# Performance work log

Hardware: AMD Instinct MI355X
Metric: run time of the kernel (lower is better)

Reference implementation:

```python
import jax, jax.numpy as jnp
import numpy as np

B, Q, A, D, H = 64, 16, 4096, 128, 8
HD = D // H
FF = 512

def _layernorm(x, g, b, eps=1e-5):
    mu = jnp.mean(x, axis=-1, keepdims=True)
    var = jnp.var(x, axis=-1, keepdims=True)
    return (x - mu) * jax.lax.rsqrt(var + eps) * g + b

def setup_inputs() -> dict:
    key = jax.random.key(0)
    ks = jax.random.split(key, 8)
    s = 0.05  # weight scale for sane numerics
    return {
        'q': jax.random.normal(ks[0], (B, Q, D), jnp.float32),
        'embed': jax.random.normal(ks[1], (B, A, D), jnp.float32),
        'attn_mask': jnp.zeros((B, Q, A), jnp.bool_),
        'batch_mask': jax.random.randint(ks[2], (B,), 0, B, jnp.int32),
        'W_kv': jax.random.normal(ks[3], (2 * D, D), jnp.float32) * s,
        'W_q': jax.random.normal(ks[4], (D, D), jnp.float32) * s,
        'W_o': jax.random.normal(ks[5], (D, D), jnp.float32) * s,
        'ln1_g': jnp.ones((D,), jnp.float32),
        'ln1_b': jnp.zeros((D,), jnp.float32),
        'ln2_g': jnp.ones((D,), jnp.float32),
        'ln2_b': jnp.zeros((D,), jnp.float32),
        'alpha1': jnp.full((1,), 0.1, jnp.float32),
        'alpha2': jnp.full((1,), 0.1, jnp.float32),
        'w_ff': jax.random.normal(ks[6], (2 * FF, D), jnp.float32) * s,
        'b_ff': jnp.zeros((2 * FF,), jnp.float32),
        'w_ff_out': jax.random.normal(ks[7], (D, FF), jnp.float32) * s,
        'b_ff_out': jnp.zeros((D,), jnp.float32),
    }

def reference(q, embed, attn_mask, batch_mask, W_kv, W_q, W_o,
              ln1_g, ln1_b, ln2_g, ln2_b, alpha1, alpha2,
              w_ff, b_ff, w_ff_out, b_ff_out):
    # cache_keys: project city embeddings to K/V, split into heads
    kv = embed @ W_kv.T                      # [B, A, 2D]
    k, v = jnp.split(kv, 2, axis=-1)
    k = k.reshape(B, A, H, HD).transpose(0, 2, 1, 3)   # [B, H, A, HD]
    v = v.reshape(B, A, H, HD).transpose(0, 2, 1, 3)   # [B, H, A, HD]

    # pre-norm query projection
    q_norm = _layernorm(q, ln1_g, ln1_b)
    gq = (q_norm @ W_q.T).reshape(B, Q, H, HD).transpose(0, 2, 1, 3)  # [B, H, Q, HD]

    # batch gather on cached K/V
    k = k[batch_mask]
    v = v[batch_mask]

    score = jnp.einsum('bhqd,bhkd->bhqk', gq, k) / jnp.sqrt(jnp.float32(HD))
    score = jnp.where(attn_mask[:, None, :, :], -jnp.inf, score)
    attn = jax.nn.softmax(score, axis=-1)
    ctx = jnp.einsum('bhqk,bhkd->bhqd', attn, v)        # [B, H, Q, HD]
    ctx = ctx.transpose(0, 2, 1, 3).reshape(B, Q, D)
    att_out = ctx @ W_o.T

    hidden = q + alpha1 * att_out
    hn = _layernorm(hidden, ln2_g, ln2_b)
    ab = hn @ w_ff.T + b_ff                              # [B, Q, 2*FF]
    a, b = jnp.split(ab, 2, axis=-1)
    h = jax.nn.silu(a) * b
    ff_out = h @ w_ff_out.T + b_ff_out
    return hidden + alpha2 * ff_out
```

## Files before the change

### kernel.cpp

```cpp
#include <hip/hip_runtime.h>
#include <cstdint>
#include <cstddef>

#define B_ 64
#define Q_ 16
#define A_ 4096
#define D_ 128
#define H_ 8
#define HD_ 16
#define FF_ 512
#define NCHUNK 8
#define CHUNK 512
#define GQ_SCALE 0.36067376022224085f

typedef __attribute__((ext_vector_type(4))) float f32x4;
typedef __attribute__((ext_vector_type(8))) __bf16 bf16x8;
typedef __attribute__((ext_vector_type(4))) short s16x4;

static __device__ __forceinline__ short f2bf(float f) {
    __bf16 h = (__bf16)f;
    return __builtin_bit_cast(short, h);
}

static __device__ __forceinline__ f32x4 mfma32(bf16x8 a, bf16x8 b, f32x4 c) {
    return __builtin_amdgcn_mfma_f32_16x16x32_bf16(a, b, c, 0, 0, 0);
}

static __device__ __forceinline__ bf16x8 wfrag_load(const float* p) {
    float4 a = *(const float4*)p;
    float4 b = *(const float4*)(p + 4);
    bf16x8 r;
    r[0]=(__bf16)a.x; r[1]=(__bf16)a.y; r[2]=(__bf16)a.z; r[3]=(__bf16)a.w;
    r[4]=(__bf16)b.x; r[5]=(__bf16)b.y; r[6]=(__bf16)b.z; r[7]=(__bf16)b.w;
    return r;
}

__global__ __launch_bounds__(128) void kgq(
    const float* __restrict__ qin, const float* __restrict__ g1,
    const float* __restrict__ b1, const float* __restrict__ Wq,
    short* __restrict__ gq)
{
    __shared__ float sx[128];
    __shared__ float red[2];
    int r = blockIdx.x;
    int t = threadIdx.x;
    float x = qin[(size_t)r * 128 + t];
    float v = x;
    for (int o = 32; o > 0; o >>= 1) v += __shfl_down(v, o);
    if ((t & 63) == 0) red[t >> 6] = v;
    __syncthreads();
    float mu = (red[0] + red[1]) * (1.f / 128.f);
    __syncthreads();
    float d = x - mu;
    v = d * d;
    for (int o = 32; o > 0; o >>= 1) v += __shfl_down(v, o);
    if ((t & 63) == 0) red[t >> 6] = v;
    __syncthreads();
    float var = (red[0] + red[1]) * (1.f / 128.f);
    float xn = d * rsqrtf(var + 1e-5f) * g1[t] + b1[t];
    sx[t] = xn;
    __syncthreads();
    float acc = 0.f;
    const float4* wr = (const float4*)(Wq + (size_t)t * 128);
    const float4* xv = (const float4*)sx;
    for (int i = 0; i < 32; ++i) {
        float4 a = wr[i], bb = xv[i];
        acc += a.x * bb.x + a.y * bb.y + a.z * bb.z + a.w * bb.w;
    }
    gq[(size_t)r * 128 + t] = f2bf(acc * GQ_SCALE);
}

__global__ __launch_bounds__(256, 2) void kattn(
    const float* __restrict__ embed, const int* __restrict__ bmask,
    const unsigned char* __restrict__ amask, const float* __restrict__ Wkv,
    const short* __restrict__ gq, float* __restrict__ pml,
    float* __restrict__ pctx)
{
    __shared__ __align__(16) short lds[32768];
    const int KR  = 8192;
    const int VR  = 16384;
    const int PR  = 24576;
    const int MK  = 28672;

    const int chunk = blockIdx.x;
    const int b     = blockIdx.y;
    const int t = threadIdx.x;
    const int w = t >> 6;
    const int l = t & 63;
    const int g = l >> 4;
    const int c = l & 15;
    const int s = bmask[b];
    const int a0 = chunk * CHUNK;

    {
        unsigned char* mlb = (unsigned char*)&lds[MK];
        int qr = t >> 5, off = (t & 31) * 16;
        for (int p = 0; p < 2; ++p) {
            int qq = qr + p * 8;
            *(uint4*)&mlb[qq * 512 + off] =
                *(const uint4*)&amask[((size_t)(b * 16 + qq)) * 4096 + a0 + off];
        }
    }

    const bool kw = (w < 2);
    const int wrow0 = kw ? (w * 64) : (128 + (w - 2) * 64);
    bf16x8 wf[4][4];
    for (int xf = 0; xf < 4; ++xf)
        for (int kf = 0; kf < 4; ++kf)
            wf[xf][kf] = wfrag_load(Wkv + (size_t)(wrow0 + xf * 16 + c) * 128
                                        + kf * 32 + g * 8);

    bf16x8 gqA[2];
    for (int hh = 0; hh < 2; ++hh) {
        int h = 2 * w + hh;
        if (g < 2)
            gqA[hh] = *(const bf16x8*)(const void*)
                      (gq + ((size_t)(b * 16 + c)) * 128 + h * 16 + g * 8);
        else {
            bf16x8 z = {};
            gqA[hh] = z;
        }
    }

    f32x4 ctx[2];
    float mrun[2][4], lrun[2][4];
    for (int hh = 0; hh < 2; ++hh)
        for (int r = 0; r < 4; ++r) {
            ctx[hh][r] = 0.f; mrun[hh][r] = -3.0e38f; lrun[hh][r] = 0.f;
        }

    const float* esrc = embed + ((size_t)s * 4096 + a0) * 128;
    const int srow = t >> 5;
    const int scol = (t & 31) * 4;

    float4 pf[8];
    auto loadregs = [&](int ts) {
        for (int p = 0; p < 8; ++p) {
            int rr = srow + p * 8;
            pf[p] = *(const float4*)(esrc + (size_t)(ts * 64 + rr) * 128 + scol);
        }
    };
    loadregs(0);

    for (int ts = 0; ts < 8; ++ts) {
        __syncthreads();
        for (int p = 0; p < 8; ++p) {
            int rr = srow + p * 8;
            int byte = (rr * 256 + scol * 2) ^ ((rr & 7) << 4);
            s16x4 pk;
            pk[0] = f2bf(pf[p].x); pk[1] = f2bf(pf[p].y);
            pk[2] = f2bf(pf[p].z); pk[3] = f2bf(pf[p].w);
            *(s16x4*)(void*)((char*)lds + byte) = pk;
        }
        if (ts < 7) loadregs(ts + 1);
        __syncthreads();
        for (int kb4 = 0; kb4 < 4; ++kb4) {
            bf16x8 eb[4];
            for (int kf = 0; kf < 4; ++kf) {
                int rr = kb4 * 16 + c;
                int byte = (rr * 256 + kf * 64 + g * 16) ^ ((rr & 7) << 4);
                eb[kf] = *(const bf16x8*)(const void*)((char*)lds + byte);
            }
            for (int xf = 0; xf < 4; ++xf) {
                f32x4 acc = {0.f, 0.f, 0.f, 0.f};
                if (kw) { for (int kf = 0; kf < 4; ++kf) acc = mfma32(wf[xf][kf], eb[kf], acc); }
                else    { for (int kf = 0; kf < 4; ++kf) acc = mfma32(eb[kf], wf[xf][kf], acc); }
                s16x4 pk;
                pk[0] = f2bf(acc[0]); pk[1] = f2bf(acc[1]);
                pk[2] = f2bf(acc[2]); pk[3] = f2bf(acc[3]);
                if (kw) {
                    int h = w * 4 + xf;
                    int e = (h * 4 + kb4) * 256 + (g >> 1) * 128 + c * 8 + (g & 1) * 4;
                    *(s16x4*)(void*)&lds[KR + e] = pk;
                } else {
                    int h = (w - 2) * 4 + xf;
                    int e = (h * 2 + (kb4 >> 1)) * 512
                          + ((2 * (kb4 & 1) + (g >> 1)) * 16 + c) * 8 + (g & 1) * 4;
                    *(s16x4*)(void*)&lds[VR + e] = pk;
                }
            }
        }
        __syncthreads();
        float mb[4][4];
        {
            const unsigned char* mlb = (const unsigned char*)&lds[MK];
            for (int kb = 0; kb < 4; ++kb)
                for (int r = 0; r < 4; ++r)
                    mb[kb][r] = mlb[(4 * g + r) * 512 + ts * 64 + kb * 16 + c]
                                ? -1.0e30f : 0.0f;
        }
        for (int hh = 0; hh < 2; ++hh) {
            int h = 2 * w + hh;
            f32x4 sc[4];
            for (int kb = 0; kb < 4; ++kb) {
                bf16x8 kB = *(const bf16x8*)(const void*)
                            &lds[KR + (h * 4 + kb) * 256 + (g * 16 + c) * 8];
                f32x4 z = {0.f, 0.f, 0.f, 0.f};
                sc[kb] = mfma32(gqA[hh], kB, z);
            }
            float al[4], rs[4];
            for (int r = 0; r < 4; ++r) {
                float s0 = sc[0][r] + mb[0][r], s1 = sc[1][r] + mb[1][r];
                float s2 = sc[2][r] + mb[2][r], s3 = sc[3][r] + mb[3][r];
                sc[0][r] = s0; sc[1][r] = s1; sc[2][r] = s2; sc[3][r] = s3;
                float tm = fmaxf(fmaxf(s0, s1), fmaxf(s2, s3));
                for (int o = 1; o < 16; o <<= 1) tm = fmaxf(tm, __shfl_xor(tm, o));
                float mn = fmaxf(mrun[hh][r], tm);
                al[r] = exp2f(mrun[hh][r] - mn);
                mrun[hh][r] = mn;
            }
            for (int r = 0; r < 4; ++r) {
                float p0 = exp2f(sc[0][r] - mrun[hh][r]);
                float p1 = exp2f(sc[1][r] - mrun[hh][r]);
                float p2 = exp2f(sc[2][r] - mrun[hh][r]);
                float p3 = exp2f(sc[3][r] - mrun[hh][r]);
                sc[0][r] = p0; sc[1][r] = p1; sc[2][r] = p2; sc[3][r] = p3;
                float qsum = p0 + p1 + p2 + p3;
                for (int o = 1; o < 16; o <<= 1) qsum += __shfl_xor(qsum, o);
                rs[r] = qsum;
            }
            for (int r = 0; r < 4; ++r) {
                lrun[hh][r] = lrun[hh][r] * al[r] + rs[r];
                ctx[hh][r] *= al[r];
            }
            for (int kb = 0; kb < 4; ++kb) {
                int base = PR + w * 1024 + (kb >> 1) * 512;
                int khi = 2 * (kb & 1) + (c >> 3);
                for (int r = 0; r < 4; ++r)
                    lds[base + (khi * 16 + 4 * g + r) * 8 + (c & 7)] = f2bf(sc[kb][r]);
            }
            for (int k2 = 0; k2 < 2; ++k2) {
                bf16x8 pA = *(const bf16x8*)(const void*)
                            &lds[PR + w * 1024 + k2 * 512 + (g * 16 + c) * 8];
                bf16x8 vB = *(const bf16x8*)(const void*)
                            &lds[VR + (h * 2 + k2) * 512 + (g * 16 + c) * 8];
                ctx[hh] = mfma32(pA, vB, ctx[hh]);
            }
        }
    }
    for (int hh = 0; hh < 2; ++hh) {
        int h = 2 * w + hh;
        size_t base = (((size_t)b * 8 + h) * 8 + chunk) * 16;
        for (int r = 0; r < 4; ++r)
            pctx[(base + 4 * g + r) * 16 + c] = ctx[hh][r];
        if (c == 0) {
            for (int r = 0; r < 4; ++r) {
                pml[(base + 4 * g + r) * 2 + 0] = mrun[hh][r];
                pml[(base + 4 * g + r) * 2 + 1] = lrun[hh][r];
            }
        }
    }
}

__global__ __launch_bounds__(128) void kcomb(
    const float* __restrict__ pml, const float* __restrict__ pctx,
    const float* __restrict__ Wo, const float* __restrict__ qin,
    const float* __restrict__ alpha1, const float* __restrict__ g2,
    const float* __restrict__ b2, float* __restrict__ hidden,
    short* __restrict__ hn)
{
    __shared__ float scx[128];
    __shared__ float red[2];
    int r = blockIdx.x;
    int b = r >> 4, qq = r & 15;
    int d = threadIdx.x;
    int h = d >> 4, vd = d & 15;
    size_t mlb = (((size_t)b * 8 + h) * 8) * 32 + qq * 2;
    float M = -3.0e38f;
    for (int cc = 0; cc < 8; ++cc) M = fmaxf(M, pml[mlb + cc * 32]);
    float L = 0.f, cx = 0.f;
    for (int cc = 0; cc < 8; ++cc) {
        float mm = pml[mlb + cc * 32], ll = pml[mlb + cc * 32 + 1];
        float f = exp2f(mm - M);
        L += ll * f;
        cx += pctx[((((size_t)b * 8 + h) * 8 + cc) * 16 + qq) * 16 + vd] * f;
    }
    cx /= L;
    scx[d] = cx;
    __syncthreads();
    float ao = 0.f;
    const float4* wo = (const float4*)(Wo + (size_t)d * 128);
    const float4* xv = (const float4*)scx;
    for (int i = 0; i < 32; ++i) {
        float4 a = wo[i], bb = xv[i];
        ao += a.x * bb.x + a.y * bb.y + a.z * bb.z + a.w * bb.w;
    }
    float hid = qin[(size_t)r * 128 + d] + alpha1[0] * ao;
    hidden[(size_t)r * 128 + d] = hid;
    float v = hid;
    for (int o = 32; o > 0; o >>= 1) v += __shfl_down(v, o);
    if ((d & 63) == 0) red[d >> 6] = v;
    __syncthreads();
    float mu = (red[0] + red[1]) * (1.f / 128.f);
    __syncthreads();
    float dd = hid - mu;
    v = dd * dd;
    for (int o = 32; o > 0; o >>= 1) v += __shfl_down(v, o);
    if ((d & 63) == 0) red[d >> 6] = v;
    __syncthreads();
    float var = (red[0] + red[1]) * (1.f / 128.f);
    hn[(size_t)r * 128 + d] = f2bf(dd * rsqrtf(var + 1e-5f) * g2[d] + b2[d]);
}

__global__ __launch_bounds__(256) void kff(
    const short* __restrict__ hn, const float* __restrict__ wff,
    const float* __restrict__ bff, const float* __restrict__ wffo,
    float* __restrict__ ffp)
{
    __shared__ float abm[2][16][132];
    __shared__ __align__(16) short hm[16 * 136];
    int b = blockIdx.x >> 2, jt = blockIdx.x & 3;
    int t = threadIdx.x, w = t >> 6, l = t & 63, g = l >> 4, c = l & 15;
    (void)l;
    bf16x8 ha[4];
    for (int kf = 0; kf < 4; ++kf)
        ha[kf] = *(const bf16x8*)(const void*)
                 (hn + ((size_t)b * 16 + c) * 128 + kf * 32 + g * 8);
    int isb = w >> 1, colb = (w & 1) * 64;
    for (int nf = 0; nf < 4; ++nf) {
        f32x4 acc = {0.f, 0.f, 0.f, 0.f};
        int lcol = colb + nf * 16 + c;
        int wrow = isb * 512 + jt * 128 + lcol;
        for (int kf = 0; kf < 4; ++kf) {
            bf16x8 wb = wfrag_load(wff + (size_t)wrow * 128 + kf * 32 + g * 8);
            acc = mfma32(ha[kf], wb, acc);
        }
        float bias = bff[wrow];
        for (int r = 0; r < 4; ++r) abm[isb][4 * g + r][lcol] = acc[r] + bias;
    }
    __syncthreads();
    for (int it = 0; it < 8; ++it) {
        int e = it * 256 + t, qq = e >> 7, jj = e & 127;
        float a = abm[0][qq][jj], bb = abm[1][qq][jj];
        float hv = a * bb / (1.f + __expf(-a));
        hm[qq * 136 + jj] = f2bf(hv);
    }
    __syncthreads();
    bf16x8 hf[4];
    for (int kf = 0; kf < 4; ++kf)
        hf[kf] = *(const bf16x8*)(const void*)&hm[c * 136 + kf * 32 + g * 8];
    for (int nf = 0; nf < 2; ++nf) {
        f32x4 a2 = {0.f, 0.f, 0.f, 0.f};
        int dout = w * 32 + nf * 16 + c;
        for (int kf = 0; kf < 4; ++kf) {
            bf16x8 wb = wfrag_load(wffo + (size_t)dout * 512 + jt * 128
                                        + kf * 32 + g * 8);
            a2 = mfma32(hf[kf], wb, a2);
        }
        for (int r = 0; r < 4; ++r)
            ffp[((size_t)jt * 1024 + b * 16 + 4 * g + r) * 128 + dout] = a2[r];
    }
}

__global__ __launch_bounds__(256) void kout(
    const float* __restrict__ hidden, const float* __restrict__ ffp,
    const float* __restrict__ bffo, const float* __restrict__ alpha2,
    float* __restrict__ out)
{
    int i = blockIdx.x * 256 + threadIdx.x;
    float f = ffp[i] + ffp[131072 + i] + ffp[262144 + i] + ffp[393216 + i]
            + bffo[i & 127];
    out[i] = hidden[i] + alpha2[0] * f;
}

extern "C" void kernel_launch(void* const* d_in, const int* in_sizes, int n_in,
                              void* d_out, int out_size, void* d_ws, size_t ws_size,
                              hipStream_t stream)
{
    (void)in_sizes; (void)n_in; (void)out_size; (void)ws_size;
    const float* qin   = (const float*)d_in[0];
    const float* embed = (const float*)d_in[1];
    const unsigned char* amask = (const unsigned char*)d_in[2];
    const int*   bmask = (const int*)d_in[3];
    const float* Wkv   = (const float*)d_in[4];
    const float* Wq    = (const float*)d_in[5];
    const float* Wo    = (const float*)d_in[6];
    const float* g1    = (const float*)d_in[7];
    const float* b1    = (const float*)d_in[8];
    const float* g2    = (const float*)d_in[9];
    const float* b2    = (const float*)d_in[10];
    const float* al1   = (const float*)d_in[11];
    const float* al2   = (const float*)d_in[12];
    const float* wff   = (const float*)d_in[13];
    const float* bff   = (const float*)d_in[14];
    const float* wffo  = (const float*)d_in[15];
    const float* bffo  = (const float*)d_in[16];
    float* out = (float*)d_out;

    char* ws = (char*)d_ws;
    short* gqb  = (short*)(ws + 0);
    short* hnb  = (short*)(ws + 262144);
    float* hid  = (float*)(ws + 524288);
    float* pml  = (float*)(ws + 1048576);
    float* pctx = (float*)(ws + 1572864);
    float* ffp  = (float*)(ws + 5767168);

    kgq  <<<dim3(1024),   dim3(128), 0, stream>>>(qin, g1, b1, Wq, gqb);
    kattn<<<dim3(8, 64),  dim3(256), 0, stream>>>(embed, bmask, amask, Wkv,
                                                  gqb, pml, pctx);
    kcomb<<<dim3(1024),   dim3(128), 0, stream>>>(pml, pctx, Wo, qin, al1,
                                                  g2, b2, hid, hnb);
    kff  <<<dim3(256),    dim3(256), 0, stream>>>(hnb, wff, bff, wffo, ffp);
    kout <<<dim3(512),    dim3(256), 0, stream>>>(hid, ffp, bffo, al2, out);
}
```

Before: 274.7 us.

## Pre-convert weights to bf16, widen attention blocks, fuse combine/FFN/output tail

Adds a prep kernel that converts all weight matrices to bf16 once per call, so the consumer kernels no longer redo the fp32-to-bf16 conversion per fragment. The attention kernel goes to 512 threads, with one wave per head and smaller per-thread register and prefetch state. The split-softmax combine, Wo projection, second layernorm, both FFN matmuls and the output epilogue are merged into a single 64-block tail kernel, removing the global round-trips for hidden, hn and the FFN partial sums. The trade-off is that the tail runs on only 64 blocks, and there is one extra small kernel launch.

```diff
diff --git a/kernel.cpp b/kernel.cpp
--- a/kernel.cpp
+++ b/kernel.cpp
@@ -9,8 +9,6 @@
 #define H_ 8
 #define HD_ 16
 #define FF_ 512
-#define NCHUNK 8
-#define CHUNK 512
 #define GQ_SCALE 0.36067376022224085f
 
 typedef __attribute__((ext_vector_type(4))) float f32x4;
@@ -26,13 +24,22 @@
     return __builtin_amdgcn_mfma_f32_16x16x32_bf16(a, b, c, 0, 0, 0);
 }
 
-static __device__ __forceinline__ bf16x8 wfrag_load(const float* p) {
-    float4 a = *(const float4*)p;
-    float4 b = *(const float4*)(p + 4);
-    bf16x8 r;
-    r[0]=(__bf16)a.x; r[1]=(__bf16)a.y; r[2]=(__bf16)a.z; r[3]=(__bf16)a.w;
-    r[4]=(__bf16)b.x; r[5]=(__bf16)b.y; r[6]=(__bf16)b.z; r[7]=(__bf16)b.w;
-    return r;
+__global__ __launch_bounds__(256) void kprep(
+    const float* __restrict__ wkv, const float* __restrict__ wo,
+    const float* __restrict__ wff, const float* __restrict__ wffo,
+    short* __restrict__ o_kv, short* __restrict__ o_wo,
+    short* __restrict__ o_ff, short* __restrict__ o_ffo)
+{
+    int i = (blockIdx.x * 256 + threadIdx.x) * 4;
+    const float* src; short* dst; int off;
+    if (i < 32768)       { src = wkv;  dst = o_kv;  off = i; }
+    else if (i < 49152)  { src = wo;   dst = o_wo;  off = i - 32768; }
+    else if (i < 180224) { src = wff;  dst = o_ff;  off = i - 49152; }
+    else                 { src = wffo; dst = o_ffo; off = i - 180224; }
+    float4 v = *(const float4*)(src + off);
+    s16x4 p;
+    p[0] = f2bf(v.x); p[1] = f2bf(v.y); p[2] = f2bf(v.z); p[3] = f2bf(v.w);
+    *(s16x4*)(dst + off) = p;
 }
 
 __global__ __launch_bounds__(128) void kgq(
@@ -70,17 +77,17 @@
     gq[(size_t)r * 128 + t] = f2bf(acc * GQ_SCALE);
 }
 
-__global__ __launch_bounds__(256, 2) void kattn(
+__global__ __launch_bounds__(512, 4) void kattn(
     const float* __restrict__ embed, const int* __restrict__ bmask,
-    const unsigned char* __restrict__ amask, const float* __restrict__ Wkv,
+    const unsigned char* __restrict__ amask, const short* __restrict__ wkv16,
     const short* __restrict__ gq, float* __restrict__ pml,
     float* __restrict__ pctx)
 {
-    __shared__ __align__(16) short lds[32768];
+    __shared__ __align__(16) short lds[36864];
     const int KR  = 8192;
     const int VR  = 16384;
     const int PR  = 24576;
-    const int MK  = 28672;
+    const int MK  = 32768;
 
     const int chunk = blockIdx.x;
     const int b     = blockIdx.y;
@@ -90,62 +97,50 @@
     const int g = l >> 4;
     const int c = l & 15;
     const int s = bmask[b];
-    const int a0 = chunk * CHUNK;
+    const int a0 = chunk * 512;
 
     {
         unsigned char* mlb = (unsigned char*)&lds[MK];
         int qr = t >> 5, off = (t & 31) * 16;
-        for (int p = 0; p < 2; ++p) {
-            int qq = qr + p * 8;
-            *(uint4*)&mlb[qq * 512 + off] =
-                *(const uint4*)&amask[((size_t)(b * 16 + qq)) * 4096 + a0 + off];
-        }
-    }
-
-    const bool kw = (w < 2);
-    const int wrow0 = kw ? (w * 64) : (128 + (w - 2) * 64);
-    bf16x8 wf[4][4];
-    for (int xf = 0; xf < 4; ++xf)
+        *(uint4*)&mlb[qr * 512 + off] =
+            *(const uint4*)&amask[((size_t)(b * 16 + qr)) * 4096 + a0 + off];
+    }
+
+    const bool kw = (w < 4);
+    const int wrow0 = kw ? (w * 32) : (128 + (w - 4) * 32);
+    bf16x8 wf[2][4];
+    for (int xf = 0; xf < 2; ++xf)
         for (int kf = 0; kf < 4; ++kf)
-            wf[xf][kf] = wfrag_load(Wkv + (size_t)(wrow0 + xf * 16 + c) * 128
-                                        + kf * 32 + g * 8);
-
-    bf16x8 gqA[2];
-    for (int hh = 0; hh < 2; ++hh) {
-        int h = 2 * w + hh;
-        if (g < 2)
-            gqA[hh] = *(const bf16x8*)(const void*)
-                      (gq + ((size_t)(b * 16 + c)) * 128 + h * 16 + g * 8);
-        else {
-            bf16x8 z = {};
-            gqA[hh] = z;
-        }
-    }
-
-    f32x4 ctx[2];
-    float mrun[2][4], lrun[2][4];
-    for (int hh = 0; hh < 2; ++hh)
-        for (int r = 0; r < 4; ++r) {
-            ctx[hh][r] = 0.f; mrun[hh][r] = -3.0e38f; lrun[hh][r] = 0.f;
-        }
+            wf[xf][kf] = *(const bf16x8*)(const void*)
+                         (wkv16 + (size_t)(wrow0 + xf * 16 + c) * 128
+                                + kf * 32 + g * 8);
+
+    bf16x8 gqA;
+    if (g < 2)
+        gqA = *(const bf16x8*)(const void*)
+              (gq + ((size_t)(b * 16 + c)) * 128 + w * 16 + g * 8);
+    else { bf16x8 z = {}; gqA = z; }
+
+    f32x4 ctx = {0.f, 0.f, 0.f, 0.f};
+    float mrun[4], lrun[4];
+    for (int r = 0; r < 4; ++r) { mrun[r] = -3.0e38f; lrun[r] = 0.f; }
 
     const float* esrc = embed + ((size_t)s * 4096 + a0) * 128;
     const int srow = t >> 5;
     const int scol = (t & 31) * 4;
 
-    float4 pf[8];
+    float4 pf[4];
     auto loadregs = [&](int ts) {
-        for (int p = 0; p < 8; ++p) {
-            int rr = srow + p * 8;
-            pf[p] = *(const float4*)(esrc + (size_t)(ts * 64 + rr) * 128 + scol);
-        }
+        for (int p = 0; p < 4; ++p)
+            pf[p] = *(const float4*)(esrc + (size_t)(ts * 64 + srow + p * 16) * 128
+                                     + scol);
     };
     loadregs(0);
 
     for (int ts = 0; ts < 8; ++ts) {
         __syncthreads();
-        for (int p = 0; p < 8; ++p) {
-            int rr = srow + p * 8;
+        for (int p = 0; p < 4; ++p) {
+            int rr = srow + p * 16;
             int byte = (rr * 256 + scol * 2) ^ ((rr & 7) << 4);
             s16x4 pk;
             pk[0] = f2bf(pf[p].x); pk[1] = f2bf(pf[p].y);
@@ -161,7 +156,7 @@
                 int byte = (rr * 256 + kf * 64 + g * 16) ^ ((rr & 7) << 4);
                 eb[kf] = *(const bf16x8*)(const void*)((char*)lds + byte);
             }
-            for (int xf = 0; xf < 4; ++xf) {
+            for (int xf = 0; xf < 2; ++xf) {
                 f32x4 acc = {0.f, 0.f, 0.f, 0.f};
                 if (kw) { for (int kf = 0; kf < 4; ++kf) acc = mfma32(wf[xf][kf], eb[kf], acc); }
                 else    { for (int kf = 0; kf < 4; ++kf) acc = mfma32(eb[kf], wf[xf][kf], acc); }
@@ -169,11 +164,11 @@
                 pk[0] = f2bf(acc[0]); pk[1] = f2bf(acc[1]);
                 pk[2] = f2bf(acc[2]); pk[3] = f2bf(acc[3]);
                 if (kw) {
-                    int h = w * 4 + xf;
+                    int h = 2 * w + xf;
                     int e = (h * 4 + kb4) * 256 + (g >> 1) * 128 + c * 8 + (g & 1) * 4;
                     *(s16x4*)(void*)&lds[KR + e] = pk;
                 } else {
-                    int h = (w - 2) * 4 + xf;
+                    int h = 2 * (w - 4) + xf;
                     int e = (h * 2 + (kb4 >> 1)) * 512
                           + ((2 * (kb4 & 1) + (g >> 1)) * 16 + c) * 8 + (g & 1) * 4;
                     *(s16x4*)(void*)&lds[VR + e] = pk;
@@ -189,178 +184,195 @@
                     mb[kb][r] = mlb[(4 * g + r) * 512 + ts * 64 + kb * 16 + c]
                                 ? -1.0e30f : 0.0f;
         }
-        for (int hh = 0; hh < 2; ++hh) {
-            int h = 2 * w + hh;
-            f32x4 sc[4];
-            for (int kb = 0; kb < 4; ++kb) {
-                bf16x8 kB = *(const bf16x8*)(const void*)
-                            &lds[KR + (h * 4 + kb) * 256 + (g * 16 + c) * 8];
-                f32x4 z = {0.f, 0.f, 0.f, 0.f};
-                sc[kb] = mfma32(gqA[hh], kB, z);
-            }
-            float al[4], rs[4];
-            for (int r = 0; r < 4; ++r) {
-                float s0 = sc[0][r] + mb[0][r], s1 = sc[1][r] + mb[1][r];
-                float s2 = sc[2][r] + mb[2][r], s3 = sc[3][r] + mb[3][r];
-                sc[0][r] = s0; sc[1][r] = s1; sc[2][r] = s2; sc[3][r] = s3;
-                float tm = fmaxf(fmaxf(s0, s1), fmaxf(s2, s3));
-                for (int o = 1; o < 16; o <<= 1) tm = fmaxf(tm, __shfl_xor(tm, o));
-                float mn = fmaxf(mrun[hh][r], tm);
-                al[r] = exp2f(mrun[hh][r] - mn);
-                mrun[hh][r] = mn;
-            }
-            for (int r = 0; r < 4; ++r) {
-                float p0 = exp2f(sc[0][r] - mrun[hh][r]);
-                float p1 = exp2f(sc[1][r] - mrun[hh][r]);
-                float p2 = exp2f(sc[2][r] - mrun[hh][r]);
-                float p3 = exp2f(sc[3][r] - mrun[hh][r]);
-                sc[0][r] = p0; sc[1][r] = p1; sc[2][r] = p2; sc[3][r] = p3;
-                float qsum = p0 + p1 + p2 + p3;
-                for (int o = 1; o < 16; o <<= 1) qsum += __shfl_xor(qsum, o);
-                rs[r] = qsum;
-            }
-            for (int r = 0; r < 4; ++r) {
-                lrun[hh][r] = lrun[hh][r] * al[r] + rs[r];
-                ctx[hh][r] *= al[r];
-            }
-            for (int kb = 0; kb < 4; ++kb) {
-                int base = PR + w * 1024 + (kb >> 1) * 512;
-                int khi = 2 * (kb & 1) + (c >> 3);
-                for (int r = 0; r < 4; ++r)
-                    lds[base + (khi * 16 + 4 * g + r) * 8 + (c & 7)] = f2bf(sc[kb][r]);
-            }
-            for (int k2 = 0; k2 < 2; ++k2) {
-                bf16x8 pA = *(const bf16x8*)(const void*)
-                            &lds[PR + w * 1024 + k2 * 512 + (g * 16 + c) * 8];
-                bf16x8 vB = *(const bf16x8*)(const void*)
-                            &lds[VR + (h * 2 + k2) * 512 + (g * 16 + c) * 8];
-                ctx[hh] = mfma32(pA, vB, ctx[hh]);
-            }
-        }
-    }
-    for (int hh = 0; hh < 2; ++hh) {
-        int h = 2 * w + hh;
-        size_t base = (((size_t)b * 8 + h) * 8 + chunk) * 16;
-        for (int r = 0; r < 4; ++r)
-            pctx[(base + 4 * g + r) * 16 + c] = ctx[hh][r];
-        if (c == 0) {
-            for (int r = 0; r < 4; ++r) {
-                pml[(base + 4 * g + r) * 2 + 0] = mrun[hh][r];
-                pml[(base + 4 * g + r) * 2 + 1] = lrun[hh][r];
-            }
-        }
-    }
-}
-
-__global__ __launch_bounds__(128) void kcomb(
+        f32x4 sc[4];
+        for (int kb = 0; kb < 4; ++kb) {
+            bf16x8 kB = *(const bf16x8*)(const void*)
+                        &lds[KR + (w * 4 + kb) * 256 + (g * 16 + c) * 8];
+            f32x4 z = {0.f, 0.f, 0.f, 0.f};
+            sc[kb] = mfma32(gqA, kB, z);
+        }
+        float al[4], rs[4];
+        for (int r = 0; r < 4; ++r) {
+            float s0 = sc[0][r] + mb[0][r], s1 = sc[1][r] + mb[1][r];
+            float s2 = sc[2][r] + mb[2][r], s3 = sc[3][r] + mb[3][r];
+            sc[0][r] = s0; sc[1][r] = s1; sc[2][r] = s2; sc[3][r] = s3;
+            float tm = fmaxf(fmaxf(s0, s1), fmaxf(s2, s3));
+            for (int o = 1; o < 16; o <<= 1) tm = fmaxf(tm, __shfl_xor(tm, o));
+            float mn = fmaxf(mrun[r], tm);
+            al[r] = exp2f(mrun[r] - mn);
+            mrun[r] = mn;
+        }
+        for (int r = 0; r < 4; ++r) {
+            float p0 = exp2f(sc[0][r] - mrun[r]);
+            float p1 = exp2f(sc[1][r] - mrun[r]);
+            float p2 = exp2f(sc[2][r] - mrun[r]);
+            float p3 = exp2f(sc[3][r] - mrun[r]);
+            sc[0][r] = p0; sc[1][r] = p1; sc[2][r] = p2; sc[3][r] = p3;
+            float qsum = p0 + p1 + p2 + p3;
+            for (int o = 1; o < 16; o <<= 1) qsum += __shfl_xor(qsum, o);
+            rs[r] = qsum;
+        }
+        for (int r = 0; r < 4; ++r) {
+            lrun[r] = lrun[r] * al[r] + rs[r];
+            ctx[r] *= al[r];
+        }
+        for (int kb = 0; kb < 4; ++kb) {
+            int base = PR + w * 1024 + (kb >> 1) * 512;
+            int khi = 2 * (kb & 1) + (c >> 3);
+            for (int r = 0; r < 4; ++r)
+                lds[base + (khi * 16 + 4 * g + r) * 8 + (c & 7)] = f2bf(sc[kb][r]);
+        }
+        for (int k2 = 0; k2 < 2; ++k2) {
+            bf16x8 pA = *(const bf16x8*)(const void*)
+                        &lds[PR + w * 1024 + k2 * 512 + (g * 16 + c) * 8];
+            bf16x8 vB = *(const bf16x8*)(const void*)
+                        &lds[VR + (w * 2 + k2) * 512 + (g * 16 + c) * 8];
+            ctx = mfma32(pA, vB, ctx);
+        }
+    }
+    size_t base = (((size_t)b * 8 + w) * 8 + chunk) * 16;
+    for (int r = 0; r < 4; ++r)
+        pctx[(base + 4 * g + r) * 16 + c] = ctx[r];
+    if (c == 0) {
+        for (int r = 0; r < 4; ++r) {
+            pml[(base + 4 * g + r) * 2 + 0] = mrun[r];
+            pml[(base + 4 * g + r) * 2 + 1] = lrun[r];
+        }
+    }
+}
+
+__global__ __launch_bounds__(256, 2) void ktail(
     const float* __restrict__ pml, const float* __restrict__ pctx,
-    const float* __restrict__ Wo, const float* __restrict__ qin,
+    const short* __restrict__ wo16, const float* __restrict__ qin,
     const float* __restrict__ alpha1, const float* __restrict__ g2,
-    const float* __restrict__ b2, float* __restrict__ hidden,
-    short* __restrict__ hn)
-{
-    __shared__ float scx[128];
-    __shared__ float red[2];
-    int r = blockIdx.x;
-    int b = r >> 4, qq = r & 15;
-    int d = threadIdx.x;
-    int h = d >> 4, vd = d & 15;
-    size_t mlb = (((size_t)b * 8 + h) * 8) * 32 + qq * 2;
-    float M = -3.0e38f;
-    for (int cc = 0; cc < 8; ++cc) M = fmaxf(M, pml[mlb + cc * 32]);
-    float L = 0.f, cx = 0.f;
-    for (int cc = 0; cc < 8; ++cc) {
-        float mm = pml[mlb + cc * 32], ll = pml[mlb + cc * 32 + 1];
-        float f = exp2f(mm - M);
-        L += ll * f;
-        cx += pctx[((((size_t)b * 8 + h) * 8 + cc) * 16 + qq) * 16 + vd] * f;
-    }
-    cx /= L;
-    scx[d] = cx;
-    __syncthreads();
-    float ao = 0.f;
-    const float4* wo = (const float4*)(Wo + (size_t)d * 128);
-    const float4* xv = (const float4*)scx;
-    for (int i = 0; i < 32; ++i) {
-        float4 a = wo[i], bb = xv[i];
-        ao += a.x * bb.x + a.y * bb.y + a.z * bb.z + a.w * bb.w;
-    }
-    float hid = qin[(size_t)r * 128 + d] + alpha1[0] * ao;
-    hidden[(size_t)r * 128 + d] = hid;
-    float v = hid;
-    for (int o = 32; o > 0; o >>= 1) v += __shfl_down(v, o);
-    if ((d & 63) == 0) red[d >> 6] = v;
-    __syncthreads();
-    float mu = (red[0] + red[1]) * (1.f / 128.f);
-    __syncthreads();
-    float dd = hid - mu;
-    v = dd * dd;
-    for (int o = 32; o > 0; o >>= 1) v += __shfl_down(v, o);
-    if ((d & 63) == 0) red[d >> 6] = v;
-    __syncthreads();
-    float var = (red[0] + red[1]) * (1.f / 128.f);
-    hn[(size_t)r * 128 + d] = f2bf(dd * rsqrtf(var + 1e-5f) * g2[d] + b2[d]);
-}
-
-__global__ __launch_bounds__(256) void kff(
-    const short* __restrict__ hn, const float* __restrict__ wff,
-    const float* __restrict__ bff, const float* __restrict__ wffo,
-    float* __restrict__ ffp)
-{
-    __shared__ float abm[2][16][132];
-    __shared__ __align__(16) short hm[16 * 136];
-    int b = blockIdx.x >> 2, jt = blockIdx.x & 3;
-    int t = threadIdx.x, w = t >> 6, l = t & 63, g = l >> 4, c = l & 15;
-    (void)l;
-    bf16x8 ha[4];
-    for (int kf = 0; kf < 4; ++kf)
-        ha[kf] = *(const bf16x8*)(const void*)
-                 (hn + ((size_t)b * 16 + c) * 128 + kf * 32 + g * 8);
-    int isb = w >> 1, colb = (w & 1) * 64;
-    for (int nf = 0; nf < 4; ++nf) {
-        f32x4 acc = {0.f, 0.f, 0.f, 0.f};
-        int lcol = colb + nf * 16 + c;
-        int wrow = isb * 512 + jt * 128 + lcol;
-        for (int kf = 0; kf < 4; ++kf) {
-            bf16x8 wb = wfrag_load(wff + (size_t)wrow * 128 + kf * 32 + g * 8);
-            acc = mfma32(ha[kf], wb, acc);
-        }
-        float bias = bff[wrow];
-        for (int r = 0; r < 4; ++r) abm[isb][4 * g + r][lcol] = acc[r] + bias;
-    }
-    __syncthreads();
-    for (int it = 0; it < 8; ++it) {
-        int e = it * 256 + t, qq = e >> 7, jj = e & 127;
-        float a = abm[0][qq][jj], bb = abm[1][qq][jj];
-        float hv = a * bb / (1.f + __expf(-a));
-        hm[qq * 136 + jj] = f2bf(hv);
-    }
-    __syncthreads();
-    bf16x8 hf[4];
-    for (int kf = 0; kf < 4; ++kf)
-        hf[kf] = *(const bf16x8*)(const void*)&hm[c * 136 + kf * 32 + g * 8];
-    for (int nf = 0; nf < 2; ++nf) {
-        f32x4 a2 = {0.f, 0.f, 0.f, 0.f};
-        int dout = w * 32 + nf * 16 + c;
-        for (int kf = 0; kf < 4; ++kf) {
-            bf16x8 wb = wfrag_load(wffo + (size_t)dout * 512 + jt * 128
-                                        + kf * 32 + g * 8);
-            a2 = mfma32(hf[kf], wb, a2);
-        }
-        for (int r = 0; r < 4; ++r)
-            ffp[((size_t)jt * 1024 + b * 16 + 4 * g + r) * 128 + dout] = a2[r];
-    }
-}
-
-__global__ __launch_bounds__(256) void kout(
-    const float* __restrict__ hidden, const float* __restrict__ ffp,
+    const float* __restrict__ b2, const short* __restrict__ wff16,
+    const float* __restrict__ bff, const short* __restrict__ wffo16,
     const float* __restrict__ bffo, const float* __restrict__ alpha2,
     float* __restrict__ out)
 {
-    int i = blockIdx.x * 256 + threadIdx.x;
-    float f = ffp[i] + ffp[131072 + i] + ffp[262144 + i] + ffp[393216 + i]
-            + bffo[i & 127];
-    out[i] = hidden[i] + alpha2[0] * f;
+    __shared__ __align__(16) short sctx[2048];
+    __shared__ __align__(16) float shid[2048];
+    __shared__ __align__(16) short shn[2048];
+    __shared__ __align__(16) short shm[8192];
+    const int b = blockIdx.x;
+    const int t = threadIdx.x;
+    const int w = t >> 6, l = t & 63, g = l >> 4, c = l & 15;
+    (void)l;
+
+    {
+        int hq = t >> 1, vh = t & 1;
+        int h = hq >> 4, qq = hq & 15;
+        const float* pm = pml + (((size_t)b * 8 + h) * 8) * 32 + qq * 2;
+        float M = -3.0e38f;
+        for (int cc = 0; cc < 8; ++cc) M = fmaxf(M, pm[cc * 32]);
+        float L = 0.f;
+        float cx[8] = {0.f,0.f,0.f,0.f,0.f,0.f,0.f,0.f};
+        for (int cc = 0; cc < 8; ++cc) {
+            float f = exp2f(pm[cc * 32] - M);
+            L += pm[cc * 32 + 1] * f;
+            const float* pc = pctx + ((((size_t)b * 8 + h) * 8 + cc) * 16 + qq) * 16
+                            + vh * 8;
+            for (int j = 0; j < 8; ++j) cx[j] += pc[j] * f;
+        }
+        float inv = 1.f / L;
+        s16x4 p0, p1;
+        for (int j = 0; j < 4; ++j) p0[j] = f2bf(cx[j] * inv);
+        for (int j = 0; j < 4; ++j) p1[j] = f2bf(cx[4 + j] * inv);
+        int off = (h * 2 + vh) * 128 + qq * 8;
+        *(s16x4*)&sctx[off] = p0;
+        *(s16x4*)&sctx[off + 4] = p1;
+    }
+    __syncthreads();
+    {
+        float a1 = alpha1[0];
+        bf16x8 cA[4];
+        for (int kf = 0; kf < 4; ++kf)
+            cA[kf] = *(const bf16x8*)(const void*)&sctx[(kf * 4 + g) * 128 + c * 8];
+        for (int nf = 0; nf < 2; ++nf) {
+            int dcol = w * 32 + nf * 16 + c;
+            f32x4 acc = {0.f, 0.f, 0.f, 0.f};
+            for (int kf = 0; kf < 4; ++kf) {
+                bf16x8 wB = *(const bf16x8*)(const void*)
+                            (wo16 + (size_t)dcol * 128 + kf * 32 + g * 8);
+                acc = mfma32(cA[kf], wB, acc);
+            }
+            for (int r = 0; r < 4; ++r) {
+                int q = 4 * g + r;
+                float hid = qin[((size_t)b * 16 + q) * 128 + dcol] + a1 * acc[r];
+                shid[q * 128 + dcol] = hid;
+            }
+        }
+    }
+    __syncthreads();
+    {
+        int row = t >> 4, ln = t & 15;
+        float x[8], sum = 0.f, sq = 0.f;
+        for (int j = 0; j < 8; ++j) {
+            x[j] = shid[row * 128 + ln * 8 + j];
+            sum += x[j]; sq += x[j] * x[j];
+        }
+        for (int o = 1; o < 16; o <<= 1) {
+            sum += __shfl_xor(sum, o);
+            sq  += __shfl_xor(sq, o);
+        }
+        float mu = sum * (1.f / 128.f);
+        float var = sq * (1.f / 128.f) - mu * mu;
+        float rstd = rsqrtf(var + 1e-5f);
+        s16x4 h0, h1;
+        for (int j = 0; j < 4; ++j)
+            h0[j] = f2bf((x[j] - mu) * rstd * g2[ln * 8 + j] + b2[ln * 8 + j]);
+        for (int j = 0; j < 4; ++j)
+            h1[j] = f2bf((x[4 + j] - mu) * rstd * g2[ln * 8 + 4 + j] + b2[ln * 8 + 4 + j]);
+        int off = ln * 128 + row * 8;
+        *(s16x4*)&shn[off] = h0;
+        *(s16x4*)&shn[off + 4] = h1;
+    }
+    __syncthreads();
+    {
+        bf16x8 hA[4];
+        for (int kf = 0; kf < 4; ++kf)
+            hA[kf] = *(const bf16x8*)(const void*)&shn[(kf * 4 + g) * 128 + c * 8];
+        for (int nf = 0; nf < 8; ++nf) {
+            int arow = w * 128 + nf * 16 + c;
+            int brow = 512 + arow;
+            f32x4 aa = {0.f,0.f,0.f,0.f}, ab = {0.f,0.f,0.f,0.f};
+            for (int kf = 0; kf < 4; ++kf) {
+                bf16x8 wa = *(const bf16x8*)(const void*)
+                            (wff16 + (size_t)arow * 128 + kf * 32 + g * 8);
+                bf16x8 wb = *(const bf16x8*)(const void*)
+                            (wff16 + (size_t)brow * 128 + kf * 32 + g * 8);
+                aa = mfma32(hA[kf], wa, aa);
+                ab = mfma32(hA[kf], wb, ab);
+            }
+            float ba = bff[arow], bb2 = bff[brow];
+            for (int r = 0; r < 4; ++r) {
+                float a = aa[r] + ba, bb = ab[r] + bb2;
+                float hv = a * bb / (1.f + __expf(-a));
+                shm[(arow >> 3) * 128 + (4 * g + r) * 8 + (c & 7)] = f2bf(hv);
+            }
+        }
+    }
+    __syncthreads();
+    {
+        float a2 = alpha2[0];
+        for (int nf = 0; nf < 2; ++nf) {
+            int dcol = w * 32 + nf * 16 + c;
+            f32x4 acc = {0.f, 0.f, 0.f, 0.f};
+            for (int kf = 0; kf < 16; ++kf) {
+                bf16x8 hA = *(const bf16x8*)(const void*)
+                            &shm[(kf * 4 + g) * 128 + c * 8];
+                bf16x8 wB = *(const bf16x8*)(const void*)
+                            (wffo16 + (size_t)dcol * 512 + kf * 32 + g * 8);
+                acc = mfma32(hA, wB, acc);
+            }
+            float bo = bffo[dcol];
+            for (int r = 0; r < 4; ++r) {
+                int q = 4 * g + r;
+                out[((size_t)b * 16 + q) * 128 + dcol] =
+                    shid[q * 128 + dcol] + a2 * (acc[r] + bo);
+            }
+        }
+    }
 }
 
 extern "C" void kernel_launch(void* const* d_in, const int* in_sizes, int n_in,
@@ -388,18 +400,20 @@
     float* out = (float*)d_out;
 
     char* ws = (char*)d_ws;
-    short* gqb  = (short*)(ws + 0);
-    short* hnb  = (short*)(ws + 262144);
-    float* hid  = (float*)(ws + 524288);
-    float* pml  = (float*)(ws + 1048576);
-    float* pctx = (float*)(ws + 1572864);
-    float* ffp  = (float*)(ws + 5767168);
-
-    kgq  <<<dim3(1024),   dim3(128), 0, stream>>>(qin, g1, b1, Wq, gqb);
-    kattn<<<dim3(8, 64),  dim3(256), 0, stream>>>(embed, bmask, amask, Wkv,
-                                                  gqb, pml, pctx);
-    kcomb<<<dim3(1024),   dim3(128), 0, stream>>>(pml, pctx, Wo, qin, al1,
-                                                  g2, b2, hid, hnb);
-    kff  <<<dim3(256),    dim3(256), 0, stream>>>(hnb, wff, bff, wffo, ffp);
-    kout <<<dim3(512),    dim3(256), 0, stream>>>(hid, ffp, bffo, al2, out);
-}
+    short* gqb    = (short*)(ws + 0);
+    float* pml    = (float*)(ws + 262144);
+    float* pctx   = (float*)(ws + 786432);
+    short* wkv16  = (short*)(ws + 4980736);
+    short* wo16   = (short*)(ws + 5046272);
+    short* wff16  = (short*)(ws + 5079040);
+    short* wffo16 = (short*)(ws + 5341184);
+
+    kprep<<<dim3(240),   dim3(256), 0, stream>>>(Wkv, Wo, wff, wffo,
+                                                 wkv16, wo16, wff16, wffo16);
+    kgq  <<<dim3(1024),  dim3(128), 0, stream>>>(qin, g1, b1, Wq, gqb);
+    kattn<<<dim3(8, 64), dim3(512), 0, stream>>>(embed, bmask, amask, wkv16,
+                                                 gqb, pml, pctx);
+    ktail<<<dim3(64),    dim3(256), 0, stream>>>(pml, pctx, wo16, qin, al1,
+                                                 g2, b2, wff16, bff, wffo16,
+                                                 bffo, al2, out);
+}
```

New measurement: 271.8 us. About the same (-1.1%).
